# Optimization experiments

Hardware: AMD Instinct MI355X
Metric: run time of the kernel (lower is better)

## Reference

```python
import jax, jax.numpy as jnp
import numpy as np

EPS = 1e-8

def spatial_similarity(x):
    # x: [B, C, H, W] -> similarity [B, 1, HW, HW]
    b, c = x.shape[0], x.shape[1]
    fm = x.reshape(b, c, -1)                                   # [B, C, HW]
    norm_fm = fm / (jnp.sqrt(jnp.sum(fm * fm, axis=1, keepdims=True)) + EPS)
    s = jnp.einsum('bcn,bcm->bnm', norm_fm, norm_fm)            # [B, HW, HW]
    return s[:, None]                                           # [B, 1, HW, HW]

def l1_loss(a, b):
    return jnp.mean(jnp.abs(a - b))

def setup_inputs() -> dict:
    key = jax.random.key(0)
    k0, k1, k2, k3 = jax.random.split(key, 4)
    shape = (8, 128, 48, 48)
    return {
        'outputs0': jax.random.normal(k0, shape, dtype=jnp.float32),
        'outputs1': jax.random.normal(k1, shape, dtype=jnp.float32),
        'targets0': jax.random.normal(k2, shape, dtype=jnp.float32),
        'targets1': jax.random.normal(k3, shape, dtype=jnp.float32),
    }

def reference(outputs0, outputs1, targets0, targets1):
    # stu_ch == tea_ch -> random index slice is identity (index = 0)
    loss = l1_loss(spatial_similarity(outputs0), spatial_similarity(targets0))
    loss = loss + l1_loss(spatial_similarity(outputs1), spatial_similarity(targets1))
    return loss
```

## Files before the change

kernel.cpp:

```cpp
#include <hip/hip_runtime.h>
#include <hip/hip_bf16.h>
#include <stdint.h>

#define B_DIM 8
#define C_DIM 128
#define N_SP 2304
#define NT 18
#define NTRI 171
#define GRID_G (2 * B_DIM * NTRI)

typedef __attribute__((ext_vector_type(8))) short short8;
typedef __attribute__((ext_vector_type(4))) float f32x4;

__device__ __forceinline__ uint32_t f2bf(float f) {
    uint32_t u = __float_as_uint(f);
    return (u + 0x7fffu + ((u >> 16) & 1u)) >> 16;
}

__global__ __launch_bounds__(256) void prep_kernel(
    const float* __restrict__ x0, const float* __restrict__ x1,
    const float* __restrict__ x2, const float* __restrict__ x3,
    ushort* __restrict__ xt, float* __restrict__ rinv)
{
    __shared__ ushort stage[64 * 128];

    int bid = blockIdx.x;
    int t  = bid / 288;
    int b  = (bid / 36) % 8;
    int nb = bid % 36;
    int tid = threadIdx.x;
    int q   = tid & 3;
    int nl  = tid >> 2;
    int n   = nb * 64 + nl;
    const float* x  = t == 0 ? x0 : t == 1 ? x1 : t == 2 ? x2 : x3;
    const float* xb = x + (size_t)b * (C_DIM * N_SP) + n;
    int sw = nl & 7;

    float s = 0.f;
#pragma unroll
    for (int jj = 0; jj < 4; ++jj) {
        uint32_t w[4];
#pragma unroll
        for (int m = 0; m < 4; ++m) {
            int c = q * 32 + jj * 8 + m * 2;
            float v0 = xb[(size_t)c * N_SP];
            float v1 = xb[(size_t)(c + 1) * N_SP];
            s = fmaf(v0, v0, s);
            s = fmaf(v1, v1, s);
            w[m] = f2bf(v0) | (f2bf(v1) << 16);
        }
        int J = q * 4 + jj;
        uint4 u; u.x = w[0]; u.y = w[1]; u.z = w[2]; u.w = w[3];
        *(uint4*)&stage[nl * 128 + ((J ^ sw) * 8)] = u;
    }
    s += __shfl_xor(s, 1, 64);
    s += __shfl_xor(s, 2, 64);
    if (q == 0) rinv[(size_t)(t * 8 + b) * N_SP + n] = 1.f / (sqrtf(s) + 1e-8f);

    __syncthreads();
    ushort* dst = xt + ((size_t)(t * 8 + b) * N_SP + (size_t)nb * 64) * 128;
#pragma unroll
    for (int it = 0; it < 4; ++it)
        *(uint4*)(dst + it * 2048 + tid * 8) = *(const uint4*)(stage + it * 2048 + tid * 8);
}

#define STAGE(xsrc, h, PA, PB)                                                      \
    {                                                                               \
        const ushort* sb = (wid & 2) ? (xsrc) + (size_t)tm * 16384                  \
                                     : (xsrc) + (size_t)tn * 16384;                 \
        ushort* pp = (wid & 2) ? (PB) : (PA);                                       \
        int i0 = (wid & 1) * 8;                                                     \
        _Pragma("unroll")                                                           \
        for (int i = 0; i < 8; ++i) {                                               \
            int ii = i0 + i;                                                        \
            int col = ii * 8 + (lane >> 3);                                         \
            const ushort* src = sb + (size_t)col * 128 + (h) * 64 + (lane & 7) * 8; \
            __builtin_amdgcn_global_load_lds(                                       \
                (const __attribute__((address_space(1))) uint32_t*)src,             \
                (__attribute__((address_space(3))) uint32_t*)(pp + ii * 512),       \
                16, 0, 0);                                                          \
        }                                                                           \
    }

#define COMPUTE(ACC, PA, PB)                                                        \
    _Pragma("unroll")                                                               \
    for (int s = 0; s < 2; ++s) {                                                   \
        short8 av[4], bv[4];                                                        \
        int g = lane >> 4;                                                          \
        _Pragma("unroll")                                                           \
        for (int i = 0; i < 4; ++i) {                                               \
            int ca = wrow * 64 + i * 16 + (lane & 15);                              \
            av[i] = *(const short8*)&(PA)[ca * 64 + ((s * 4 + g) ^ (ca & 7)) * 8];  \
            int cb = wcol * 64 + i * 16 + (lane & 15);                              \
            bv[i] = *(const short8*)&(PB)[cb * 64 + ((s * 4 + g) ^ (cb & 7)) * 8];  \
        }                                                                           \
        _Pragma("unroll")                                                           \
        for (int i = 0; i < 4; ++i)                                                 \
            _Pragma("unroll")                                                       \
            for (int j = 0; j < 4; ++j)                                             \
                ACC[i][j] = __builtin_amdgcn_mfma_f32_16x16x32_bf16(                \
                    av[i], bv[j], ACC[i][j], 0, 0, 0);                              \
    }

__global__ __launch_bounds__(256, 2) void gram_kernel(
    const ushort* __restrict__ xt, const float* __restrict__ rinv,
    float* __restrict__ accum)
{
    __shared__ ushort pA[2][128 * 64];
    __shared__ ushort pB[2][128 * 64];
    __shared__ float rn[4][128];
    __shared__ float wred[4];

    int bid0 = blockIdx.x;
    int bid  = (bid0 & 7) * (GRID_G / 8) + (bid0 >> 3);

    int pair = bid / (B_DIM * NTRI);
    int rem  = bid - pair * (B_DIM * NTRI);
    int b    = rem / NTRI;
    int t    = rem - b * NTRI;
    int tn = 0, cnt = NT;
    while (t >= cnt) { t -= cnt; --cnt; ++tn; }
    int tm = tn + t;

    const ushort* xo = xt + (size_t)(pair * 8 + b) * N_SP * 128;
    const ushort* xg = xt + (size_t)((pair + 2) * 8 + b) * N_SP * 128;
    const float*  ro = rinv + (size_t)(pair * 8 + b) * N_SP;
    const float*  rg = rinv + (size_t)((pair + 2) * 8 + b) * N_SP;

    int tid  = threadIdx.x;
    int wid  = tid >> 6;
    int lane = tid & 63;
    int wrow = wid >> 1, wcol = wid & 1;

    f32x4 acc_o[4][4], acc_t[4][4];
#pragma unroll
    for (int i = 0; i < 4; ++i)
#pragma unroll
        for (int j = 0; j < 4; ++j) {
            acc_o[i][j] = (f32x4){0.f, 0.f, 0.f, 0.f};
            acc_t[i][j] = (f32x4){0.f, 0.f, 0.f, 0.f};
        }

    STAGE(xo, 0, pA[0], pB[0]);
    if (tid < 128) {
        rn[0][tid] = ro[tn * 128 + tid];
        rn[1][tid] = ro[tm * 128 + tid];
    } else {
        int q = tid - 128;
        rn[2][q] = rg[tn * 128 + q];
        rn[3][q] = rg[tm * 128 + q];
    }
    __syncthreads();
    STAGE(xo, 1, pA[1], pB[1]);
    COMPUTE(acc_o, pA[0], pB[0]);
    __syncthreads();
    STAGE(xg, 0, pA[0], pB[0]);
    COMPUTE(acc_o, pA[1], pB[1]);
    __syncthreads();
    STAGE(xg, 1, pA[1], pB[1]);
    COMPUTE(acc_t, pA[0], pB[0]);
    __syncthreads();
    COMPUTE(acc_t, pA[1], pB[1]);

    int fr = lane & 15, fq = lane >> 4;
    float co[4], cg[4];
#pragma unroll
    for (int j = 0; j < 4; ++j) {
        co[j] = rn[1][wcol * 64 + j * 16 + fr];
        cg[j] = rn[3][wcol * 64 + j * 16 + fr];
    }
    float w2 = (tn == tm) ? 1.f : 2.f;
    float lsum = 0.f;
#pragma unroll
    for (int i = 0; i < 4; ++i) {
#pragma unroll
        for (int r = 0; r < 4; ++r) {
            int rowl = wrow * 64 + i * 16 + fq * 4 + r;
            float ror = rn[0][rowl], rgr = rn[2][rowl];
#pragma unroll
            for (int j = 0; j < 4; ++j) {
                float so = acc_o[i][j][r] * ror * co[j];
                float st = acc_t[i][j][r] * rgr * cg[j];
                lsum += fabsf(so - st);
            }
        }
    }
    lsum *= w2;
#pragma unroll
    for (int off = 32; off > 0; off >>= 1) lsum += __shfl_down(lsum, off, 64);
    if (lane == 0) wred[wid] = lsum;
    __syncthreads();
    if (tid == 0)
        atomicAdd(&accum[pair * 32 + (bid0 & 31)], wred[0] + wred[1] + wred[2] + wred[3]);
}

__global__ void finalize_kernel(const float* __restrict__ a, float* __restrict__ out) {
    float s = 0.f;
    for (int i = 0; i < 64; ++i) s += a[i];
    out[0] = s * (1.0f / 42467328.0f);
}

extern "C" void kernel_launch(void* const* d_in, const int* in_sizes, int n_in,
                              void* d_out, int out_size, void* d_ws, size_t ws_size,
                              hipStream_t stream) {
    const float* o0 = (const float*)d_in[0];
    const float* o1 = (const float*)d_in[1];
    const float* t0 = (const float*)d_in[2];
    const float* t1 = (const float*)d_in[3];

    ushort* xtw  = (ushort*)d_ws;
    float*  rinv = (float*)((char*)d_ws + (size_t)4 * 8 * N_SP * 256);
    float*  accum = rinv + 4 * 8 * N_SP;

    hipMemsetAsync(accum, 0, 64 * sizeof(float), stream);
    prep_kernel<<<1152, 256, 0, stream>>>(o0, o1, t0, t1, xtw, rinv);
    gram_kernel<<<GRID_G, 256, 0, stream>>>(xtw, rinv, accum);
    finalize_kernel<<<1, 1, 0, stream>>>(accum, (float*)d_out);
}
```

Measured before the change: 126.3 us.

## Process two tiles per gram block and overlap next tile load with epilogue

Measured after the change: 121.5 us. 1.04x faster.

```diff
diff --git a/kernel.cpp b/kernel.cpp
--- a/kernel.cpp
+++ b/kernel.cpp
@@ -7,7 +7,8 @@
 #define N_SP 2304
 #define NT 18
 #define NTRI 171
-#define GRID_G (2 * B_DIM * NTRI)
+#define NTILES (2 * B_DIM * NTRI)
+#define GRID_G (NTILES / 2)
 
 typedef __attribute__((ext_vector_type(8))) short short8;
 typedef __attribute__((ext_vector_type(4))) float f32x4;
@@ -20,11 +21,12 @@
 __global__ __launch_bounds__(256) void prep_kernel(
     const float* __restrict__ x0, const float* __restrict__ x1,
     const float* __restrict__ x2, const float* __restrict__ x3,
-    ushort* __restrict__ xt, float* __restrict__ rinv)
+    ushort* __restrict__ xt, float* __restrict__ rinv, float* __restrict__ accum)
 {
     __shared__ ushort stage[64 * 128];
 
     int bid = blockIdx.x;
+    if (bid == 0 && threadIdx.x < 64) accum[threadIdx.x] = 0.f;
     int t  = bid / 288;
     int b  = (bid / 36) % 8;
     int nb = bid % 36;
@@ -64,10 +66,34 @@
         *(uint4*)(dst + it * 2048 + tid * 8) = *(const uint4*)(stage + it * 2048 + tid * 8);
 }
 
-#define STAGE(xsrc, h, PA, PB)                                                      \
+struct TileInfo {
+    const ushort* xo; const ushort* xg;
+    const float*  ro; const float*  rg;
+    int tn, tm; float w2; int pair;
+};
+
+__device__ __forceinline__ TileInfo decode_tile(int g, const ushort* xt, const float* rinv) {
+    int pair = g / (B_DIM * NTRI);
+    int rem  = g - pair * (B_DIM * NTRI);
+    int b    = rem / NTRI;
+    int t    = rem - b * NTRI;
+    int tn = 0, cnt = NT;
+    while (t >= cnt) { t -= cnt; --cnt; ++tn; }
+    TileInfo ti;
+    ti.tn = tn; ti.tm = tn + t;
+    ti.xo = xt + (size_t)(pair * 8 + b) * N_SP * 128;
+    ti.xg = xt + (size_t)((pair + 2) * 8 + b) * N_SP * 128;
+    ti.ro = rinv + (size_t)(pair * 8 + b) * N_SP;
+    ti.rg = rinv + (size_t)((pair + 2) * 8 + b) * N_SP;
+    ti.w2 = (tn == ti.tm) ? 1.f : 2.f;
+    ti.pair = pair;
+    return ti;
+}
+
+#define STAGE(sbase, TN, TM, h, PA, PB)                                             \
     {                                                                               \
-        const ushort* sb = (wid & 2) ? (xsrc) + (size_t)tm * 16384                  \
-                                     : (xsrc) + (size_t)tn * 16384;                 \
+        const ushort* sb = (wid & 2) ? (sbase) + (size_t)(TM) * 16384               \
+                                     : (sbase) + (size_t)(TN) * 16384;              \
         ushort* pp = (wid & 2) ? (PB) : (PA);                                       \
         int i0 = (wid & 1) * 8;                                                     \
         _Pragma("unroll")                                                           \
@@ -102,30 +128,59 @@
                     av[i], bv[j], ACC[i][j], 0, 0, 0);                              \
     }
 
+#define ZERO_ACC()                                                                  \
+    _Pragma("unroll")                                                               \
+    for (int i = 0; i < 4; ++i)                                                     \
+        _Pragma("unroll")                                                           \
+        for (int j = 0; j < 4; ++j) {                                               \
+            acc_o[i][j] = (f32x4){0.f, 0.f, 0.f, 0.f};                              \
+            acc_t[i][j] = (f32x4){0.f, 0.f, 0.f, 0.f};                              \
+        }
+
+#define EPILOGUE(Q, W2)                                                             \
+    {                                                                               \
+        int fr = lane & 15, fq = lane >> 4;                                         \
+        float co[4], cg[4];                                                         \
+        _Pragma("unroll")                                                           \
+        for (int j = 0; j < 4; ++j) {                                               \
+            co[j] = rn[Q][1][wcol * 64 + j * 16 + fr];                              \
+            cg[j] = rn[Q][3][wcol * 64 + j * 16 + fr];                              \
+        }                                                                           \
+        float lsum = 0.f;                                                           \
+        _Pragma("unroll")                                                           \
+        for (int i = 0; i < 4; ++i) {                                               \
+            _Pragma("unroll")                                                       \
+            for (int r = 0; r < 4; ++r) {                                           \
+                int rowl = wrow * 64 + i * 16 + fq * 4 + r;                         \
+                float ror = rn[Q][0][rowl], rgr = rn[Q][2][rowl];                   \
+                _Pragma("unroll")                                                   \
+                for (int j = 0; j < 4; ++j) {                                       \
+                    float so = acc_o[i][j][r] * ror * co[j];                        \
+                    float st = acc_t[i][j][r] * rgr * cg[j];                        \
+                    lsum += fabsf(so - st);                                         \
+                }                                                                   \
+            }                                                                       \
+        }                                                                           \
+        lsum *= (W2);                                                               \
+        _Pragma("unroll")                                                           \
+        for (int off = 32; off > 0; off >>= 1) lsum += __shfl_down(lsum, off, 64);  \
+        if (lane == 0) wred[wid] = lsum;                                            \
+    }
+
 __global__ __launch_bounds__(256, 2) void gram_kernel(
     const ushort* __restrict__ xt, const float* __restrict__ rinv,
     float* __restrict__ accum)
 {
     __shared__ ushort pA[2][128 * 64];
     __shared__ ushort pB[2][128 * 64];
-    __shared__ float rn[4][128];
+    __shared__ float rn[2][4][128];
     __shared__ float wred[4];
 
     int bid0 = blockIdx.x;
     int bid  = (bid0 & 7) * (GRID_G / 8) + (bid0 >> 3);
 
-    int pair = bid / (B_DIM * NTRI);
-    int rem  = bid - pair * (B_DIM * NTRI);
-    int b    = rem / NTRI;
-    int t    = rem - b * NTRI;
-    int tn = 0, cnt = NT;
-    while (t >= cnt) { t -= cnt; --cnt; ++tn; }
-    int tm = tn + t;
-
-    const ushort* xo = xt + (size_t)(pair * 8 + b) * N_SP * 128;
-    const ushort* xg = xt + (size_t)((pair + 2) * 8 + b) * N_SP * 128;
-    const float*  ro = rinv + (size_t)(pair * 8 + b) * N_SP;
-    const float*  rg = rinv + (size_t)((pair + 2) * 8 + b) * N_SP;
+    TileInfo t0 = decode_tile(2 * bid,     xt, rinv);
+    TileInfo t1 = decode_tile(2 * bid + 1, xt, rinv);
 
     int tid  = threadIdx.x;
     int wid  = tid >> 6;
@@ -133,71 +188,61 @@
     int wrow = wid >> 1, wcol = wid & 1;
 
     f32x4 acc_o[4][4], acc_t[4][4];
-#pragma unroll
-    for (int i = 0; i < 4; ++i)
-#pragma unroll
-        for (int j = 0; j < 4; ++j) {
-            acc_o[i][j] = (f32x4){0.f, 0.f, 0.f, 0.f};
-            acc_t[i][j] = (f32x4){0.f, 0.f, 0.f, 0.f};
-        }
-
-    STAGE(xo, 0, pA[0], pB[0]);
+    ZERO_ACC();
+
+    STAGE(t0.xo, t0.tn, t0.tm, 0, pA[0], pB[0]);
     if (tid < 128) {
-        rn[0][tid] = ro[tn * 128 + tid];
-        rn[1][tid] = ro[tm * 128 + tid];
+        rn[0][0][tid] = t0.ro[t0.tn * 128 + tid];
+        rn[0][1][tid] = t0.ro[t0.tm * 128 + tid];
+        rn[1][0][tid] = t1.ro[t1.tn * 128 + tid];
+        rn[1][1][tid] = t1.ro[t1.tm * 128 + tid];
     } else {
-        int q = tid - 128;
-        rn[2][q] = rg[tn * 128 + q];
-        rn[3][q] = rg[tm * 128 + q];
-    }
-    __syncthreads();
-    STAGE(xo, 1, pA[1], pB[1]);
+        int u = tid - 128;
+        rn[0][2][u] = t0.rg[t0.tn * 128 + u];
+        rn[0][3][u] = t0.rg[t0.tm * 128 + u];
+        rn[1][2][u] = t1.rg[t1.tn * 128 + u];
+        rn[1][3][u] = t1.rg[t1.tm * 128 + u];
+    }
+    __syncthreads();
+    STAGE(t0.xo, t0.tn, t0.tm, 1, pA[1], pB[1]);
     COMPUTE(acc_o, pA[0], pB[0]);
     __syncthreads();
-    STAGE(xg, 0, pA[0], pB[0]);
+    STAGE(t0.xg, t0.tn, t0.tm, 0, pA[0], pB[0]);
     COMPUTE(acc_o, pA[1], pB[1]);
     __syncthreads();
-    STAGE(xg, 1, pA[1], pB[1]);
+    STAGE(t0.xg, t0.tn, t0.tm, 1, pA[1], pB[1]);
     COMPUTE(acc_t, pA[0], pB[0]);
     __syncthreads();
+    STAGE(t1.xo, t1.tn, t1.tm, 0, pA[0], pB[0]);
     COMPUTE(acc_t, pA[1], pB[1]);
-
-    int fr = lane & 15, fq = lane >> 4;
-    float co[4], cg[4];
-#pragma unroll
-    for (int j = 0; j < 4; ++j) {
-        co[j] = rn[1][wcol * 64 + j * 16 + fr];
-        cg[j] = rn[3][wcol * 64 + j * 16 + fr];
-    }
-    float w2 = (tn == tm) ? 1.f : 2.f;
-    float lsum = 0.f;
-#pragma unroll
-    for (int i = 0; i < 4; ++i) {
-#pragma unroll
-        for (int r = 0; r < 4; ++r) {
-            int rowl = wrow * 64 + i * 16 + fq * 4 + r;
-            float ror = rn[0][rowl], rgr = rn[2][rowl];
-#pragma unroll
-            for (int j = 0; j < 4; ++j) {
-                float so = acc_o[i][j][r] * ror * co[j];
-                float st = acc_t[i][j][r] * rgr * cg[j];
-                lsum += fabsf(so - st);
-            }
-        }
-    }
-    lsum *= w2;
-#pragma unroll
-    for (int off = 32; off > 0; off >>= 1) lsum += __shfl_down(lsum, off, 64);
-    if (lane == 0) wred[wid] = lsum;
+    EPILOGUE(0, t0.w2);
+    ZERO_ACC();
     __syncthreads();
     if (tid == 0)
-        atomicAdd(&accum[pair * 32 + (bid0 & 31)], wred[0] + wred[1] + wred[2] + wred[3]);
+        atomicAdd(&accum[t0.pair * 32 + (bid0 & 31)],
+                  wred[0] + wred[1] + wred[2] + wred[3]);
+    STAGE(t1.xo, t1.tn, t1.tm, 1, pA[1], pB[1]);
+    COMPUTE(acc_o, pA[0], pB[0]);
+    __syncthreads();
+    STAGE(t1.xg, t1.tn, t1.tm, 0, pA[0], pB[0]);
+    COMPUTE(acc_o, pA[1], pB[1]);
+    __syncthreads();
+    STAGE(t1.xg, t1.tn, t1.tm, 1, pA[1], pB[1]);
+    COMPUTE(acc_t, pA[0], pB[0]);
+    __syncthreads();
+    COMPUTE(acc_t, pA[1], pB[1]);
+    EPILOGUE(1, t1.w2);
+    __syncthreads();
+    if (tid == 0)
+        atomicAdd(&accum[t1.pair * 32 + (bid0 & 31)],
+                  wred[0] + wred[1] + wred[2] + wred[3]);
 }
 
 __global__ void finalize_kernel(const float* __restrict__ a, float* __restrict__ out) {
-    float s = 0.f;
-    for (int i = 0; i < 64; ++i) s += a[i];
-    out[0] = s * (1.0f / 42467328.0f);
+    float s = a[threadIdx.x];
+#pragma unroll
+    for (int off = 32; off > 0; off >>= 1) s += __shfl_down(s, off, 64);
+    if (threadIdx.x == 0) out[0] = s * (1.0f / 42467328.0f);
 }
 
 extern "C" void kernel_launch(void* const* d_in, const int* in_sizes, int n_in,
@@ -212,8 +257,7 @@
     float*  rinv = (float*)((char*)d_ws + (size_t)4 * 8 * N_SP * 256);
     float*  accum = rinv + 4 * 8 * N_SP;
 
-    hipMemsetAsync(accum, 0, 64 * sizeof(float), stream);
-    prep_kernel<<<1152, 256, 0, stream>>>(o0, o1, t0, t1, xtw, rinv);
+    prep_kernel<<<1152, 256, 0, stream>>>(o0, o1, t0, t1, xtw, rinv, accum);
     gram_kernel<<<GRID_G, 256, 0, stream>>>(xtw, rinv, accum);
-    finalize_kernel<<<1, 1, 0, stream>>>(accum, (float*)d_out);
-}
+    finalize_kernel<<<1, 64, 0, stream>>>(accum, (float*)d_out);
+}
```

## Fold L1 difference into one concatenated-K GEMM with pre-normalized bf16 inputs

Applied to the files above, without the earlier changes.

New measurement: 238.7 us. +89.1%, slower.

```diff
diff --git a/kernel.cpp b/kernel.cpp
--- a/kernel.cpp
+++ b/kernel.cpp
@@ -7,7 +7,8 @@
 #define N_SP 2304
 #define NT 18
 #define NTRI 171
-#define GRID_G (2 * B_DIM * NTRI)
+#define NTILES (2 * B_DIM * NTRI)
+#define GRID_G (NTILES / 2)
 
 typedef __attribute__((ext_vector_type(8))) short short8;
 typedef __attribute__((ext_vector_type(4))) float f32x4;
@@ -20,15 +21,19 @@
 __global__ __launch_bounds__(256) void prep_kernel(
     const float* __restrict__ x0, const float* __restrict__ x1,
     const float* __restrict__ x2, const float* __restrict__ x3,
-    ushort* __restrict__ xt, float* __restrict__ rinv)
+    ushort* __restrict__ xcat, float* __restrict__ accum, int* __restrict__ ticket)
 {
     __shared__ ushort stage[64 * 128];
 
     int bid = blockIdx.x;
+    int tid = threadIdx.x;
+    if (bid == 0) {
+        if (tid < 64) accum[tid] = 0.f;
+        if (tid == 64) *ticket = 0;
+    }
     int t  = bid / 288;
     int b  = (bid / 36) % 8;
     int nb = bid % 36;
-    int tid = threadIdx.x;
     int q   = tid & 3;
     int nl  = tid >> 2;
     int n   = nb * 64 + nl;
@@ -36,45 +41,73 @@
     const float* xb = x + (size_t)b * (C_DIM * N_SP) + n;
     int sw = nl & 7;
 
+    float v[32];
     float s = 0.f;
+#pragma unroll
+    for (int m = 0; m < 32; ++m) {
+        v[m] = xb[(size_t)(q * 32 + m) * N_SP];
+        s = fmaf(v[m], v[m], s);
+    }
+    s += __shfl_xor(s, 1, 64);
+    s += __shfl_xor(s, 2, 64);
+    float r = 1.f / (sqrtf(s) + 1e-8f);
+
 #pragma unroll
     for (int jj = 0; jj < 4; ++jj) {
         uint32_t w[4];
 #pragma unroll
-        for (int m = 0; m < 4; ++m) {
-            int c = q * 32 + jj * 8 + m * 2;
-            float v0 = xb[(size_t)c * N_SP];
-            float v1 = xb[(size_t)(c + 1) * N_SP];
-            s = fmaf(v0, v0, s);
-            s = fmaf(v1, v1, s);
-            w[m] = f2bf(v0) | (f2bf(v1) << 16);
+        for (int m2 = 0; m2 < 4; ++m2) {
+            float a0 = v[jj * 8 + 2 * m2]     * r;
+            float a1 = v[jj * 8 + 2 * m2 + 1] * r;
+            w[m2] = f2bf(a0) | (f2bf(a1) << 16);
         }
         int J = q * 4 + jj;
         uint4 u; u.x = w[0]; u.y = w[1]; u.z = w[2]; u.w = w[3];
         *(uint4*)&stage[nl * 128 + ((J ^ sw) * 8)] = u;
     }
-    s += __shfl_xor(s, 1, 64);
-    s += __shfl_xor(s, 2, 64);
-    if (q == 0) rinv[(size_t)(t * 8 + b) * N_SP + n] = 1.f / (sqrtf(s) + 1e-8f);
-
-    __syncthreads();
-    ushort* dst = xt + ((size_t)(t * 8 + b) * N_SP + (size_t)nb * 64) * 128;
-#pragma unroll
-    for (int it = 0; it < 4; ++it)
-        *(uint4*)(dst + it * 2048 + tid * 8) = *(const uint4*)(stage + it * 2048 + tid * 8);
-}
-
-#define STAGE(xsrc, h, PA, PB)                                                      \
+    __syncthreads();
+
+    int pair = t & 1, half = t >> 1;
+    ushort* dstbase = xcat + ((size_t)(pair * 8 + b) * N_SP + (size_t)nb * 64) * 256
+                    + half * 128;
+#pragma unroll
+    for (int it = 0; it < 4; ++it) {
+        int idx = it * 256 + tid;
+        int row = idx >> 4, c = idx & 15;
+        *(uint4*)(dstbase + (size_t)row * 256 + c * 8) =
+            *(const uint4*)(stage + row * 128 + c * 8);
+    }
+}
+
+struct TileInfo { size_t base; int tn, tm; float w2; int pair; };
+
+__device__ __forceinline__ TileInfo decode_tile(int g) {
+    int pair = g / (B_DIM * NTRI);
+    int rem  = g - pair * (B_DIM * NTRI);
+    int b    = rem / NTRI;
+    int t    = rem - b * NTRI;
+    int tn = 0, cnt = NT;
+    while (t >= cnt) { t -= cnt; --cnt; ++tn; }
+    TileInfo ti;
+    ti.tn = tn; ti.tm = tn + t;
+    ti.base = (size_t)(pair * 8 + b) * N_SP * 256;
+    ti.w2 = (tn == ti.tm) ? 1.f : 2.f;
+    ti.pair = pair;
+    return ti;
+}
+
+#define STAGE(BASE, TN, TM, HH, HL)                                                 \
     {                                                                               \
-        const ushort* sb = (wid & 2) ? (xsrc) + (size_t)tm * 16384                  \
-                                     : (xsrc) + (size_t)tn * 16384;                 \
-        ushort* pp = (wid & 2) ? (PB) : (PA);                                       \
+        const ushort* sb = xcat + (BASE) +                                          \
+            (size_t)(((wid & 2) ? (TM) : (TN)) * 128) * 256;                        \
+        ushort* pp = (wid & 2) ? pB : pA;                                           \
         int i0 = (wid & 1) * 8;                                                     \
         _Pragma("unroll")                                                           \
         for (int i = 0; i < 8; ++i) {                                               \
             int ii = i0 + i;                                                        \
             int col = ii * 8 + (lane >> 3);                                         \
-            const ushort* src = sb + (size_t)col * 128 + (h) * 64 + (lane & 7) * 8; \
+            const ushort* src = sb + (size_t)col * 256 + (HH) * 128 + (HL) * 64     \
+                              + (lane & 7) * 8;                                     \
             __builtin_amdgcn_global_load_lds(                                       \
                 (const __attribute__((address_space(1))) uint32_t*)src,             \
                 (__attribute__((address_space(3))) uint32_t*)(pp + ii * 512),       \
@@ -82,7 +115,7 @@
         }                                                                           \
     }
 
-#define COMPUTE(ACC, PA, PB)                                                        \
+#define COMPUTE(NEG)                                                                \
     _Pragma("unroll")                                                               \
     for (int s = 0; s < 2; ++s) {                                                   \
         short8 av[4], bv[4];                                                        \
@@ -90,114 +123,112 @@
         _Pragma("unroll")                                                           \
         for (int i = 0; i < 4; ++i) {                                               \
             int ca = wrow * 64 + i * 16 + (lane & 15);                              \
-            av[i] = *(const short8*)&(PA)[ca * 64 + ((s * 4 + g) ^ (ca & 7)) * 8];  \
+            av[i] = *(const short8*)&pA[ca * 64 + ((s * 4 + g) ^ (ca & 7)) * 8];    \
             int cb = wcol * 64 + i * 16 + (lane & 15);                              \
-            bv[i] = *(const short8*)&(PB)[cb * 64 + ((s * 4 + g) ^ (cb & 7)) * 8];  \
+            bv[i] = *(const short8*)&pB[cb * 64 + ((s * 4 + g) ^ (cb & 7)) * 8];    \
+            if (NEG) {                                                              \
+                _Pragma("unroll")                                                   \
+                for (int d = 0; d < 4; ++d)                                         \
+                    ((uint32_t*)&bv[i])[d] ^= 0x80008000u;                          \
+            }                                                                       \
         }                                                                           \
         _Pragma("unroll")                                                           \
         for (int i = 0; i < 4; ++i)                                                 \
             _Pragma("unroll")                                                       \
             for (int j = 0; j < 4; ++j)                                             \
-                ACC[i][j] = __builtin_amdgcn_mfma_f32_16x16x32_bf16(                \
-                    av[i], bv[j], ACC[i][j], 0, 0, 0);                              \
-    }
-
-__global__ __launch_bounds__(256, 2) void gram_kernel(
-    const ushort* __restrict__ xt, const float* __restrict__ rinv,
-    float* __restrict__ accum)
+                acc[i][j] = __builtin_amdgcn_mfma_f32_16x16x32_bf16(                \
+                    av[i], bv[j], acc[i][j], 0, 0, 0);                              \
+    }
+
+#define ZERO_ACC()                                                                  \
+    _Pragma("unroll")                                                               \
+    for (int i = 0; i < 4; ++i)                                                     \
+        _Pragma("unroll")                                                           \
+        for (int j = 0; j < 4; ++j)                                                 \
+            acc[i][j] = (f32x4){0.f, 0.f, 0.f, 0.f};
+
+#define EPILOGUE_ABS(W2, OUT)                                                       \
+    {                                                                               \
+        float lsum = 0.f;                                                           \
+        _Pragma("unroll")                                                           \
+        for (int i = 0; i < 4; ++i)                                                 \
+            _Pragma("unroll")                                                       \
+            for (int j = 0; j < 4; ++j)                                             \
+                _Pragma("unroll")                                                   \
+                for (int rr = 0; rr < 4; ++rr)                                      \
+                    lsum += fabsf(acc[i][j][rr]);                                   \
+        lsum *= (W2);                                                               \
+        _Pragma("unroll")                                                           \
+        for (int off = 32; off > 0; off >>= 1)                                      \
+            lsum += __shfl_down(lsum, off, 64);                                     \
+        OUT = lsum;                                                                 \
+    }
+
+__global__ __launch_bounds__(256, 4) void gram_kernel(
+    const ushort* __restrict__ xcat, float* __restrict__ accum,
+    int* __restrict__ ticket, float* __restrict__ out)
 {
-    __shared__ ushort pA[2][128 * 64];
-    __shared__ ushort pB[2][128 * 64];
-    __shared__ float rn[4][128];
-    __shared__ float wred[4];
+    __shared__ ushort pA[128 * 64];
+    __shared__ ushort pB[128 * 64];
+    __shared__ int lastflag;
 
     int bid0 = blockIdx.x;
     int bid  = (bid0 & 7) * (GRID_G / 8) + (bid0 >> 3);
 
-    int pair = bid / (B_DIM * NTRI);
-    int rem  = bid - pair * (B_DIM * NTRI);
-    int b    = rem / NTRI;
-    int t    = rem - b * NTRI;
-    int tn = 0, cnt = NT;
-    while (t >= cnt) { t -= cnt; --cnt; ++tn; }
-    int tm = tn + t;
-
-    const ushort* xo = xt + (size_t)(pair * 8 + b) * N_SP * 128;
-    const ushort* xg = xt + (size_t)((pair + 2) * 8 + b) * N_SP * 128;
-    const float*  ro = rinv + (size_t)(pair * 8 + b) * N_SP;
-    const float*  rg = rinv + (size_t)((pair + 2) * 8 + b) * N_SP;
+    TileInfo t0 = decode_tile(2 * bid);
+    TileInfo t1 = decode_tile(2 * bid + 1);
 
     int tid  = threadIdx.x;
     int wid  = tid >> 6;
     int lane = tid & 63;
     int wrow = wid >> 1, wcol = wid & 1;
 
-    f32x4 acc_o[4][4], acc_t[4][4];
-#pragma unroll
-    for (int i = 0; i < 4; ++i)
-#pragma unroll
-        for (int j = 0; j < 4; ++j) {
-            acc_o[i][j] = (f32x4){0.f, 0.f, 0.f, 0.f};
-            acc_t[i][j] = (f32x4){0.f, 0.f, 0.f, 0.f};
-        }
-
-    STAGE(xo, 0, pA[0], pB[0]);
-    if (tid < 128) {
-        rn[0][tid] = ro[tn * 128 + tid];
-        rn[1][tid] = ro[tm * 128 + tid];
-    } else {
-        int q = tid - 128;
-        rn[2][q] = rg[tn * 128 + q];
-        rn[3][q] = rg[tm * 128 + q];
-    }
-    __syncthreads();
-    STAGE(xo, 1, pA[1], pB[1]);
-    COMPUTE(acc_o, pA[0], pB[0]);
-    __syncthreads();
-    STAGE(xg, 0, pA[0], pB[0]);
-    COMPUTE(acc_o, pA[1], pB[1]);
-    __syncthreads();
-    STAGE(xg, 1, pA[1], pB[1]);
-    COMPUTE(acc_t, pA[0], pB[0]);
-    __syncthreads();
-    COMPUTE(acc_t, pA[1], pB[1]);
-
-    int fr = lane & 15, fq = lane >> 4;
-    float co[4], cg[4];
-#pragma unroll
-    for (int j = 0; j < 4; ++j) {
-        co[j] = rn[1][wcol * 64 + j * 16 + fr];
-        cg[j] = rn[3][wcol * 64 + j * 16 + fr];
-    }
-    float w2 = (tn == tm) ? 1.f : 2.f;
-    float lsum = 0.f;
-#pragma unroll
-    for (int i = 0; i < 4; ++i) {
-#pragma unroll
-        for (int r = 0; r < 4; ++r) {
-            int rowl = wrow * 64 + i * 16 + fq * 4 + r;
-            float ror = rn[0][rowl], rgr = rn[2][rowl];
-#pragma unroll
-            for (int j = 0; j < 4; ++j) {
-                float so = acc_o[i][j][r] * ror * co[j];
-                float st = acc_t[i][j][r] * rgr * cg[j];
-                lsum += fabsf(so - st);
-            }
-        }
-    }
-    lsum *= w2;
-#pragma unroll
-    for (int off = 32; off > 0; off >>= 1) lsum += __shfl_down(lsum, off, 64);
-    if (lane == 0) wred[wid] = lsum;
-    __syncthreads();
-    if (tid == 0)
-        atomicAdd(&accum[pair * 32 + (bid0 & 31)], wred[0] + wred[1] + wred[2] + wred[3]);
-}
-
-__global__ void finalize_kernel(const float* __restrict__ a, float* __restrict__ out) {
-    float s = 0.f;
-    for (int i = 0; i < 64; ++i) s += a[i];
-    out[0] = s * (1.0f / 42467328.0f);
+    f32x4 acc[4][4];
+    ZERO_ACC();
+    float sum0, sum1;
+
+    STAGE(t0.base, t0.tn, t0.tm, 0, 0); __syncthreads();
+    COMPUTE(0);                         __syncthreads();
+    STAGE(t0.base, t0.tn, t0.tm, 0, 1); __syncthreads();
+    COMPUTE(0);                         __syncthreads();
+    STAGE(t0.base, t0.tn, t0.tm, 1, 0); __syncthreads();
+    COMPUTE(1);                         __syncthreads();
+    STAGE(t0.base, t0.tn, t0.tm, 1, 1); __syncthreads();
+    COMPUTE(1);                         __syncthreads();
+
+    STAGE(t1.base, t1.tn, t1.tm, 0, 0);
+    EPILOGUE_ABS(t0.w2, sum0);
+    ZERO_ACC();
+    __syncthreads();
+    COMPUTE(0);                         __syncthreads();
+    STAGE(t1.base, t1.tn, t1.tm, 0, 1); __syncthreads();
+    COMPUTE(0);                         __syncthreads();
+    STAGE(t1.base, t1.tn, t1.tm, 1, 0); __syncthreads();
+    COMPUTE(1);                         __syncthreads();
+    STAGE(t1.base, t1.tn, t1.tm, 1, 1); __syncthreads();
+    COMPUTE(1);
+    EPILOGUE_ABS(t1.w2, sum1);
+
+    if (lane == 0) {
+        atomicAdd(&accum[t0.pair * 32 + (bid0 & 31)], sum0);
+        atomicAdd(&accum[t1.pair * 32 + (bid0 & 31)], sum1);
+    }
+
+    __syncthreads();
+    if (tid == 0) {
+        __threadfence();
+        int old = __hip_atomic_fetch_add(ticket, 1, __ATOMIC_ACQ_REL,
+                                         __HIP_MEMORY_SCOPE_AGENT);
+        lastflag = (old == GRID_G - 1);
+    }
+    __syncthreads();
+    if (lastflag && tid < 64) {
+        float s2 = __hip_atomic_load(&accum[tid], __ATOMIC_RELAXED,
+                                     __HIP_MEMORY_SCOPE_AGENT);
+#pragma unroll
+        for (int off = 32; off > 0; off >>= 1) s2 += __shfl_down(s2, off, 64);
+        if (tid == 0) out[0] = s2 * (1.0f / 42467328.0f);
+    }
 }
 
 extern "C" void kernel_launch(void* const* d_in, const int* in_sizes, int n_in,
@@ -208,12 +239,10 @@
     const float* t0 = (const float*)d_in[2];
     const float* t1 = (const float*)d_in[3];
 
-    ushort* xtw  = (ushort*)d_ws;
-    float*  rinv = (float*)((char*)d_ws + (size_t)4 * 8 * N_SP * 256);
-    float*  accum = rinv + 4 * 8 * N_SP;
-
-    hipMemsetAsync(accum, 0, 64 * sizeof(float), stream);
-    prep_kernel<<<1152, 256, 0, stream>>>(o0, o1, t0, t1, xtw, rinv);
-    gram_kernel<<<GRID_G, 256, 0, stream>>>(xtw, rinv, accum);
-    finalize_kernel<<<1, 1, 0, stream>>>(accum, (float*)d_out);
-}
+    ushort* xcat  = (ushort*)d_ws;
+    float*  accum = (float*)((char*)d_ws + (size_t)2 * 8 * N_SP * 512);
+    int*    ticket = (int*)(accum + 128);
+
+    prep_kernel<<<1152, 256, 0, stream>>>(o0, o1, t0, t1, xcat, accum, ticket);
+    gram_kernel<<<GRID_G, 256, 0, stream>>>(xcat, accum, ticket, (float*)d_out);
+}
```

## Single-buffer gram LDS for higher occupancy, fold memset into prep, parallel finalize

Applied to the files above, without the earlier changes.

After: 149.3 us. 1.18x slower.

```diff
diff --git a/kernel.cpp b/kernel.cpp
--- a/kernel.cpp
+++ b/kernel.cpp
@@ -7,7 +7,7 @@
 #define N_SP 2304
 #define NT 18
 #define NTRI 171
-#define GRID_G (2 * B_DIM * NTRI)
+#define NTILES (2 * B_DIM * NTRI)
 
 typedef __attribute__((ext_vector_type(8))) short short8;
 typedef __attribute__((ext_vector_type(4))) float f32x4;
@@ -20,11 +20,12 @@
 __global__ __launch_bounds__(256) void prep_kernel(
     const float* __restrict__ x0, const float* __restrict__ x1,
     const float* __restrict__ x2, const float* __restrict__ x3,
-    ushort* __restrict__ xt, float* __restrict__ rinv)
+    ushort* __restrict__ xt, float* __restrict__ rinv, float* __restrict__ accum)
 {
     __shared__ ushort stage[64 * 128];
 
     int bid = blockIdx.x;
+    if (bid == 0 && threadIdx.x < 64) accum[threadIdx.x] = 0.f;
     int t  = bid / 288;
     int b  = (bid / 36) % 8;
     int nb = bid % 36;
@@ -64,11 +65,11 @@
         *(uint4*)(dst + it * 2048 + tid * 8) = *(const uint4*)(stage + it * 2048 + tid * 8);
 }
 
-#define STAGE(xsrc, h, PA, PB)                                                      \
+#define STAGE(xsrc, h)                                                              \
     {                                                                               \
         const ushort* sb = (wid & 2) ? (xsrc) + (size_t)tm * 16384                  \
                                      : (xsrc) + (size_t)tn * 16384;                 \
-        ushort* pp = (wid & 2) ? (PB) : (PA);                                       \
+        ushort* pp = (wid & 2) ? pB : pA;                                           \
         int i0 = (wid & 1) * 8;                                                     \
         _Pragma("unroll")                                                           \
         for (int i = 0; i < 8; ++i) {                                               \
@@ -82,7 +83,7 @@
         }                                                                           \
     }
 
-#define COMPUTE(ACC, PA, PB)                                                        \
+#define COMPUTE(ACC)                                                                \
     _Pragma("unroll")                                                               \
     for (int s = 0; s < 2; ++s) {                                                   \
         short8 av[4], bv[4];                                                        \
@@ -90,9 +91,9 @@
         _Pragma("unroll")                                                           \
         for (int i = 0; i < 4; ++i) {                                               \
             int ca = wrow * 64 + i * 16 + (lane & 15);                              \
-            av[i] = *(const short8*)&(PA)[ca * 64 + ((s * 4 + g) ^ (ca & 7)) * 8];  \
+            av[i] = *(const short8*)&pA[ca * 64 + ((s * 4 + g) ^ (ca & 7)) * 8];    \
             int cb = wcol * 64 + i * 16 + (lane & 15);                              \
-            bv[i] = *(const short8*)&(PB)[cb * 64 + ((s * 4 + g) ^ (cb & 7)) * 8];  \
+            bv[i] = *(const short8*)&pB[cb * 64 + ((s * 4 + g) ^ (cb & 7)) * 8];    \
         }                                                                           \
         _Pragma("unroll")                                                           \
         for (int i = 0; i < 4; ++i)                                                 \
@@ -102,17 +103,17 @@
                     av[i], bv[j], ACC[i][j], 0, 0, 0);                              \
     }
 
-__global__ __launch_bounds__(256, 2) void gram_kernel(
+__global__ __launch_bounds__(256, 4) void gram_kernel(
     const ushort* __restrict__ xt, const float* __restrict__ rinv,
     float* __restrict__ accum)
 {
-    __shared__ ushort pA[2][128 * 64];
-    __shared__ ushort pB[2][128 * 64];
+    __shared__ ushort pA[128 * 64];
+    __shared__ ushort pB[128 * 64];
     __shared__ float rn[4][128];
     __shared__ float wred[4];
 
     int bid0 = blockIdx.x;
-    int bid  = (bid0 & 7) * (GRID_G / 8) + (bid0 >> 3);
+    int bid  = (bid0 & 7) * (NTILES / 8) + (bid0 >> 3);
 
     int pair = bid / (B_DIM * NTRI);
     int rem  = bid - pair * (B_DIM * NTRI);
@@ -141,7 +142,7 @@
             acc_t[i][j] = (f32x4){0.f, 0.f, 0.f, 0.f};
         }
 
-    STAGE(xo, 0, pA[0], pB[0]);
+    STAGE(xo, 0);
     if (tid < 128) {
         rn[0][tid] = ro[tn * 128 + tid];
         rn[1][tid] = ro[tm * 128 + tid];
@@ -151,16 +152,19 @@
         rn[3][q] = rg[tm * 128 + q];
     }
     __syncthreads();
-    STAGE(xo, 1, pA[1], pB[1]);
-    COMPUTE(acc_o, pA[0], pB[0]);
-    __syncthreads();
-    STAGE(xg, 0, pA[0], pB[0]);
-    COMPUTE(acc_o, pA[1], pB[1]);
-    __syncthreads();
-    STAGE(xg, 1, pA[1], pB[1]);
-    COMPUTE(acc_t, pA[0], pB[0]);
-    __syncthreads();
-    COMPUTE(acc_t, pA[1], pB[1]);
+    COMPUTE(acc_o);
+    __syncthreads();
+    STAGE(xo, 1);
+    __syncthreads();
+    COMPUTE(acc_o);
+    __syncthreads();
+    STAGE(xg, 0);
+    __syncthreads();
+    COMPUTE(acc_t);
+    __syncthreads();
+    STAGE(xg, 1);
+    __syncthreads();
+    COMPUTE(acc_t);
 
     int fr = lane & 15, fq = lane >> 4;
     float co[4], cg[4];
@@ -195,9 +199,10 @@
 }
 
 __global__ void finalize_kernel(const float* __restrict__ a, float* __restrict__ out) {
-    float s = 0.f;
-    for (int i = 0; i < 64; ++i) s += a[i];
-    out[0] = s * (1.0f / 42467328.0f);
+    float s = a[threadIdx.x];
+#pragma unroll
+    for (int off = 32; off > 0; off >>= 1) s += __shfl_down(s, off, 64);
+    if (threadIdx.x == 0) out[0] = s * (1.0f / 42467328.0f);
 }
 
 extern "C" void kernel_launch(void* const* d_in, const int* in_sizes, int n_in,
@@ -212,8 +217,7 @@
     float*  rinv = (float*)((char*)d_ws + (size_t)4 * 8 * N_SP * 256);
     float*  accum = rinv + 4 * 8 * N_SP;
 
-    hipMemsetAsync(accum, 0, 64 * sizeof(float), stream);
-    prep_kernel<<<1152, 256, 0, stream>>>(o0, o1, t0, t1, xtw, rinv);
-    gram_kernel<<<GRID_G, 256, 0, stream>>>(xtw, rinv, accum);
-    finalize_kernel<<<1, 1, 0, stream>>>(accum, (float*)d_out);
-}
+    prep_kernel<<<1152, 256, 0, stream>>>(o0, o1, t0, t1, xtw, rinv, accum);
+    gram_kernel<<<NTILES, 256, 0, stream>>>(xtw, rinv, accum);
+    finalize_kernel<<<1, 64, 0, stream>>>(accum, (float*)d_out);
+}
```
